# Kernel optimization log

Hardware: AMD Instinct MI355X
Metric: run time of the kernel (lower is better)

The kernel has to match this reference:

```python
import jax, jax.numpy as jnp
import numpy as np

N = 100000      # nodes
E = 1600000     # edges (avg degree 16)
B = 64          # graphs in batch
DIN = 128
HID = (256, 128, 64)
EPS = 1e-5


def _gcn(x, W, b, src, dst, n):
    # GCNConv: symmetric normalization with self-loops (already appended to src/dst)
    h = x @ W                                                   # [N, out]
    deg = jax.ops.segment_sum(jnp.ones_like(dst, dtype=h.dtype), dst, num_segments=n)
    dinv = jnp.where(deg > 0, jax.lax.rsqrt(jnp.maximum(deg, 1.0)), 0.0)
    norm = dinv[src] * dinv[dst]                                # [E+N]
    msg = h[src] * norm[:, None]                                # gather + scale
    return jax.ops.segment_sum(msg, dst, num_segments=n) + b    # scatter-add


def _bn(x, g, b):
    # BatchNorm1d over nodes (batch statistics, deterministic)
    mu = x.mean(0)
    var = x.var(0)
    return (x - mu) * jax.lax.rsqrt(var + EPS) * g + b


def setup_inputs():
    key = jax.random.key(0)
    ks = jax.random.split(key, 32)
    inp = {}
    inp["x"] = jax.random.normal(ks[0], (N, DIN), jnp.float32)
    inp["edge_index"] = jax.random.randint(ks[1], (2, E), 0, N, jnp.int32)
    inp["batch"] = jnp.sort(jax.random.randint(ks[2], (N,), 0, B, jnp.int32))
    dims = [DIN] + list(HID)
    for i in range(3):
        inp[f"W{i}"] = jax.random.normal(ks[3 + 4 * i], (dims[i], dims[i + 1]), jnp.float32) / np.sqrt(dims[i]).astype(np.float32)
        inp[f"b{i}"] = jnp.zeros((dims[i + 1],), jnp.float32)
        inp[f"g{i}"] = jnp.ones((dims[i + 1],), jnp.float32)
        inp[f"be{i}"] = jnp.zeros((dims[i + 1],), jnp.float32)
    d = HID[-1]
    inp["ln_g"] = jnp.ones((d,), jnp.float32)
    inp["ln_b"] = jnp.zeros((d,), jnp.float32)
    inp["att"] = jax.random.normal(ks[15], (d, 1), jnp.float32)
    mdims = [d, d // 2, d // 4, 2]
    for i in range(3):
        inp[f"M{i}W"] = jax.random.normal(ks[16 + 2 * i], (mdims[i], mdims[i + 1]), jnp.float32) / np.sqrt(mdims[i]).astype(np.float32)
        inp[f"M{i}b"] = jnp.zeros((mdims[i + 1],), jnp.float32)
    return inp


def reference(x, edge_index, batch, W0, b0, g0, be0, W1, b1, g1, be1, W2, b2, g2, be2,
              ln_g, ln_b, att, M0W, M0b, M1W, M1b, M2W, M2b):
    n = x.shape[0]
    loop = jnp.arange(n, dtype=edge_index.dtype)
    src = jnp.concatenate([edge_index[0], loop])
    dst = jnp.concatenate([edge_index[1], loop])
    for (W, b, g, be) in ((W0, b0, g0, be0), (W1, b1, g1, be1), (W2, b2, g2, be2)):
        x = jax.nn.relu(_bn(_gcn(x, W, b, src, dst, n), g, be))
    # LayerNorm over features
    mu = x.mean(-1, keepdims=True)
    var = x.var(-1, keepdims=True)
    x = (x - mu) * jax.lax.rsqrt(var + EPS) * ln_g + ln_b
    # global attention weights (softmax over ALL nodes, as in original code)
    aw = jax.nn.softmax(jnp.tanh(x @ att), axis=0)   # [N, 1]
    x = x * aw
    # global mean pool per graph
    s = jax.ops.segment_sum(x, batch, num_segments=B)
    cnt = jax.ops.segment_sum(jnp.ones((n, 1), x.dtype), batch, num_segments=B)
    pooled = s / jnp.maximum(cnt, 1.0)               # [B, 64]
    h = jax.nn.relu(pooled @ M0W + M0b)
    h = jax.nn.relu(h @ M1W + M1b)
    return h @ M2W + M2b                             # [B, 2]
```

## Files before the change

### kernel.cpp

```cpp
#include <hip/hip_runtime.h>
#include <hip/hip_bf16.h>
#include <cstdint>
#include <cstddef>

typedef float    f32x4  __attribute__((ext_vector_type(4)));
typedef __bf16   bf16x8 __attribute__((ext_vector_type(8)));
typedef _Float16 f16x4  __attribute__((ext_vector_type(4)));
typedef _Float16 f16x8  __attribute__((ext_vector_type(8)));

#define BN_G1 1024

__device__ __forceinline__ unsigned short f2bf(float x){
  unsigned u = __float_as_uint(x);
  return (unsigned short)((u + 0x7fffu + ((u >> 16) & 1u)) >> 16);
}
__device__ __forceinline__ float bfhi(unsigned short h){
  return __uint_as_float(((unsigned)h) << 16);
}

__global__ void k_deg_hist(const int* __restrict__ dst, int* __restrict__ deg, int E,
                           unsigned long long M){
  int f   = blockIdx.x & 7;
  int cid = blockIdx.x >> 3;
  int nch = gridDim.x >> 3;
  for(int i = cid*blockDim.x + threadIdx.x; i < E; i += nch*blockDim.x){
    int d = dst[i];
    int xf = (int)(((unsigned long long)(unsigned)d * M) >> 40);
    if(xf == f) atomicAdd(&deg[d], 1);
  }
}

__global__ void k_batch_hist(const int* __restrict__ batch, int* __restrict__ cnt, int n){
  __shared__ int h[64];
  if(threadIdx.x<64) h[threadIdx.x]=0;
  __syncthreads();
  int i = blockIdx.x*blockDim.x + threadIdx.x;
  int stride = gridDim.x*blockDim.x;
  for(; i<n; i+=stride) atomicAdd(&h[batch[i]], 1);
  __syncthreads();
  if(threadIdx.x<64 && h[threadIdx.x]) atomicAdd(&cnt[threadIdx.x], h[threadIdx.x]);
}

__global__ void k_dinv(const int* __restrict__ deg, float* __restrict__ dinv, int n){
  int i = blockIdx.x*blockDim.x + threadIdx.x;
  if(i<n) dinv[i] = rsqrtf((float)(deg[i]+1));
}

__global__ void k_scan1(const int* __restrict__ deg, int* __restrict__ bsum, int n){
  __shared__ int s[256];
  int base = blockIdx.x*1024 + threadIdx.x*4;
  int acc=0;
  #pragma unroll
  for(int j=0;j<4;j++){ int i=base+j; if(i<n) acc+=deg[i]; }
  s[threadIdx.x]=acc; __syncthreads();
  for(int off=128;off>0;off>>=1){
    if(threadIdx.x<off) s[threadIdx.x]+=s[threadIdx.x+off];
    __syncthreads();
  }
  if(threadIdx.x==0) bsum[blockIdx.x]=s[0];
}

__global__ void k_scan2(int* __restrict__ bsum, int nblk, int* __restrict__ rowptr, int n){
  __shared__ int s[128];
  int t=threadIdx.x;
  int v = (t<nblk)? bsum[t] : 0;
  s[t]=v; __syncthreads();
  for(int off=1; off<128; off<<=1){
    int a = (t>=off)? s[t-off] : 0;
    __syncthreads();
    s[t]+=a;
    __syncthreads();
  }
  if(t<nblk) bsum[t]=s[t]-v;
  if(t==127) rowptr[n]=s[127];
}

__global__ void k_scan3(const int* __restrict__ deg, const int* __restrict__ bsum,
                        int* __restrict__ rowptr, int* __restrict__ cursor, int n){
  __shared__ int s[256];
  int base = blockIdx.x*1024 + threadIdx.x*4;
  int v[4]; int acc=0;
  #pragma unroll
  for(int j=0;j<4;j++){ int i=base+j; v[j]=(i<n)?deg[i]:0; acc+=v[j]; }
  s[threadIdx.x]=acc; __syncthreads();
  for(int off=1; off<256; off<<=1){
    int a = (threadIdx.x>=off)? s[threadIdx.x-off] : 0;
    __syncthreads();
    s[threadIdx.x]+=a;
    __syncthreads();
  }
  int excl = s[threadIdx.x]-acc + bsum[blockIdx.x];
  #pragma unroll
  for(int j=0;j<4;j++){
    int i=base+j;
    if(i<n){ rowptr[i]=excl; cursor[i]=excl; excl+=v[j]; }
  }
}

__global__ void k_csr_fill(const int* __restrict__ src, const int* __restrict__ dst,
                           int* __restrict__ cursor, int* __restrict__ adj, int E,
                           unsigned long long M){
  int f   = blockIdx.x & 7;
  int cid = blockIdx.x >> 3;
  int nch = gridDim.x >> 3;
  for(int i = cid*blockDim.x + threadIdx.x; i < E; i += nch*blockDim.x){
    int d = dst[i];
    int xf = (int)(((unsigned long long)(unsigned)d * M) >> 40);
    if(xf == f){
      int p = atomicAdd(&cursor[d], 1);
      adj[p] = src[i];
    }
  }
}


__global__ void k_prep_w(const float* __restrict__ W, unsigned short* __restrict__ Wh,
                         unsigned short* __restrict__ Wl, int K, int F){
  int i = blockIdx.x*256 + threadIdx.x;
  if(i < K*F){
    int k = i / F, f = i % F;
    float a = W[i];
    unsigned short h = f2bf(a);
    Wh[(size_t)f*K + k] = h;
    Wl[(size_t)f*K + k] = f2bf(a - bfhi(h));
  }
}

__global__ void k_prep_x(const float* __restrict__ x, const float* __restrict__ dinv,
                         _Float16* __restrict__ x16, int n){
  int tid = blockIdx.x*256 + threadIdx.x;
  int node = tid >> 5;
  if(node>=n) return;
  int c4 = tid & 31;
  size_t idx = ((size_t)node<<5) + c4;
  float4 v = ((const float4*)x)[idx];
  float d = dinv[node];
  f16x4 o;
  o[0]=(_Float16)(v.x*d); o[1]=(_Float16)(v.y*d); o[2]=(_Float16)(v.z*d); o[3]=(_Float16)(v.w*d);
  ((f16x4*)x16)[idx] = o;
}

__global__ void k_agg16(const _Float16* __restrict__ zs, const int* __restrict__ rowptr,
                        const int* __restrict__ adj, const float* __restrict__ dinv,
                        const float* __restrict__ bias, _Float16* __restrict__ out,
                        int n, int lg8){
  int tid = blockIdx.x*blockDim.x + threadIdx.x;
  int node = tid >> lg8;
  if(node>=n) return;
  int c8 = tid & ((1<<lg8)-1);
  const f16x8* z8 = (const f16x8*)zs;
  size_t rb = ((size_t)node<<lg8) + c8;
  f16x8 self = z8[rb];
  float a0[8], a1[8], a2[8], a3[8];
  #pragma unroll
  for(int j=0;j<8;j++){ a0[j]=(float)self[j]; a1[j]=0.f; a2[j]=0.f; a3[j]=0.f; }
  int e = rowptr[node], end = rowptr[node+1];
  for(; e+3<end; e+=4){
    int s0=adj[e], s1=adj[e+1], s2=adj[e+2], s3=adj[e+3];
    f16x8 v0 = z8[((size_t)s0<<lg8)+c8];
    f16x8 v1 = z8[((size_t)s1<<lg8)+c8];
    f16x8 v2 = z8[((size_t)s2<<lg8)+c8];
    f16x8 v3 = z8[((size_t)s3<<lg8)+c8];
    #pragma unroll
    for(int j=0;j<8;j++){
      a0[j]+=(float)v0[j]; a1[j]+=(float)v1[j];
      a2[j]+=(float)v2[j]; a3[j]+=(float)v3[j];
    }
  }
  for(; e<end; e++){
    f16x8 v0 = z8[((size_t)adj[e]<<lg8)+c8];
    #pragma unroll
    for(int j=0;j<8;j++) a0[j]+=(float)v0[j];
  }
  float di = dinv[node];
  f16x8 o;
  #pragma unroll
  for(int j=0;j<8;j++){
    float r = ((a0[j]+a1[j])+(a2[j]+a3[j]))*di;
    if(bias) r += bias[(c8<<3)+j];
    o[j] = (_Float16)r;
  }
  ((f16x8*)out)[rb] = o;
}


template<typename AT> struct AFrag;
template<> struct AFrag<float>{
  float4 a,b;
  __device__ __forceinline__ void load(const float* p){ a=*(const float4*)p; b=*(const float4*)(p+4); }
  __device__ __forceinline__ void get(float o[8]) const {
    o[0]=a.x;o[1]=a.y;o[2]=a.z;o[3]=a.w;o[4]=b.x;o[5]=b.y;o[6]=b.z;o[7]=b.w;
  }
};
template<> struct AFrag<_Float16>{
  f16x8 v;
  __device__ __forceinline__ void load(const _Float16* p){ v=*(const f16x8*)p; }
  __device__ __forceinline__ void get(float o[8]) const {
    #pragma unroll
    for(int j=0;j<8;j++) o[j]=(float)v[j];
  }
};

template<int K, int F, bool BN, bool BIAS, bool RSC, typename AT, typename OT>
__global__ __launch_bounds__(256,2) void k_gemm_mfma(const AT* __restrict__ A,
    const unsigned short* __restrict__ Bh, const unsigned short* __restrict__ Bl,
    const float* __restrict__ sc, const float* __restrict__ sh,
    const float* __restrict__ bias, const float* __restrict__ rsc,
    OT* __restrict__ C, int n){
  constexpr int NF = F/16;
  __shared__ uint4 sBh[F*4];
  __shared__ uint4 sBl[F*4];
  const int l   = threadIdx.x & 63;
  const int w   = threadIdx.x >> 6;
  const int rlo = l & 15;
  const int khi = l >> 4;
  const int row0 = blockIdx.x*128 + w*32;

  f32x4 acc[2][NF];
  #pragma unroll
  for(int i=0;i<2;i++)
    #pragma unroll
    for(int j=0;j<NF;j++) acc[i][j] = (f32x4){0.f,0.f,0.f,0.f};

  const size_t e0 = (size_t)min(row0 + rlo,      n-1) * K + khi*8;
  const size_t e1 = (size_t)min(row0 + 16 + rlo, n-1) * K + khi*8;

  AFrag<AT> c0,c1,x0f,x1f;
  c0.load(A + e0); c1.load(A + e1);

  #pragma unroll 1
  for(int k0=0; k0<K; k0+=32){
    if(k0+32 < K){
      x0f.load(A + e0 + k0 + 32);
      x1f.load(A + e1 + k0 + 32);
    }
    __syncthreads();
    #pragma unroll
    for(int j=0;j<F/64;j++){
      int i  = threadIdx.x + j*256;
      int f  = i >> 2;
      int k8 = i & 3;
      int g  = ((f>>4)<<6) + (k8<<4) + (f&15);
      size_t goff = (size_t)f*K + k0 + (k8<<3);
      sBh[g] = *(const uint4*)(Bh + goff);
      sBl[g] = *(const uint4*)(Bl + goff);
    }
    float scr[8], shr[8];
    if(BN){
      float4 s0 = *(const float4*)(sc + k0 + khi*8);
      float4 s1 = *(const float4*)(sc + k0 + khi*8 + 4);
      float4 t0 = *(const float4*)(sh + k0 + khi*8);
      float4 t1 = *(const float4*)(sh + k0 + khi*8 + 4);
      scr[0]=s0.x;scr[1]=s0.y;scr[2]=s0.z;scr[3]=s0.w;scr[4]=s1.x;scr[5]=s1.y;scr[6]=s1.z;scr[7]=s1.w;
      shr[0]=t0.x;shr[1]=t0.y;shr[2]=t0.z;shr[3]=t0.w;shr[4]=t1.x;shr[5]=t1.y;shr[6]=t1.z;shr[7]=t1.w;
    }
    union { unsigned short u[8]; bf16x8 v; } H0,L0,H1,L1;
    {
      float v0[8], v1[8];
      c0.get(v0); c1.get(v1);
      #pragma unroll
      for(int j=0;j<8;j++){
        float y0 = v0[j], y1 = v1[j];
        if(BN){ y0 = fmaxf(fmaf(y0,scr[j],shr[j]),0.f); y1 = fmaxf(fmaf(y1,scr[j],shr[j]),0.f); }
        unsigned short h0 = f2bf(y0), h1 = f2bf(y1);
        H0.u[j]=h0; L0.u[j]=f2bf(y0 - bfhi(h0));
        H1.u[j]=h1; L1.u[j]=f2bf(y1 - bfhi(h1));
      }
    }
    bf16x8 ah0=H0.v, al0=L0.v, ah1=H1.v, al1=L1.v;
    __syncthreads();
    #pragma unroll
    for(int cf=0; cf<NF; cf++){
      bf16x8 bh = ((const bf16x8*)sBh)[cf*64 + l];
      bf16x8 bl = ((const bf16x8*)sBl)[cf*64 + l];
      acc[0][cf] = __builtin_amdgcn_mfma_f32_16x16x32_bf16(ah0, bh, acc[0][cf], 0,0,0);
      acc[1][cf] = __builtin_amdgcn_mfma_f32_16x16x32_bf16(ah1, bh, acc[1][cf], 0,0,0);
      acc[0][cf] = __builtin_amdgcn_mfma_f32_16x16x32_bf16(al0, bh, acc[0][cf], 0,0,0);
      acc[1][cf] = __builtin_amdgcn_mfma_f32_16x16x32_bf16(al1, bh, acc[1][cf], 0,0,0);
      acc[0][cf] = __builtin_amdgcn_mfma_f32_16x16x32_bf16(ah0, bl, acc[0][cf], 0,0,0);
      acc[1][cf] = __builtin_amdgcn_mfma_f32_16x16x32_bf16(ah1, bl, acc[1][cf], 0,0,0);
    }
    c0=x0f; c1=x1f;
  }

  #pragma unroll
  for(int rf=0; rf<2; rf++){
    #pragma unroll
    for(int r=0; r<4; r++){
      int m = row0 + rf*16 + khi*4 + r;
      if(m < n){
        float rs = RSC ? rsc[m] : 1.f;
        #pragma unroll
        for(int cf=0; cf<NF; cf++){
          int col = rlo + 16*cf;
          float v = acc[rf][cf][r];
          if(BIAS) v += bias[col];
          v *= rs;
          C[(size_t)m*F + col] = (OT)v;
        }
      }
    }
  }
}

__global__ __launch_bounds__(256) void k_bn_stats16(const _Float16* __restrict__ h,
                            float* __restrict__ partials, int n, int lgF){
  const int F   = 1 << lgF;
  const int C8  = 1 << (lgF-3);
  const int c8  = threadIdx.x & (C8-1);
  const int sub = threadIdx.x >> (lgF-3);
  const int rpb = 256 >> (lgF-3);
  float s[8], s2[8];
  #pragma unroll
  for(int j=0;j<8;j++){ s[j]=0.f; s2[j]=0.f; }
  for(int row = blockIdx.x*rpb + sub; row < n; row += gridDim.x*rpb){
    f16x8 v = ((const f16x8*)h)[(size_t)row*C8 + c8];
    #pragma unroll
    for(int j=0;j<8;j++){ float f=(float)v[j]; s[j]+=f; s2[j]=fmaf(f,f,s2[j]); }
  }
  __shared__ float rs [256*9];
  __shared__ float rs2[256*9];
  #pragma unroll
  for(int j=0;j<8;j++){ rs[threadIdx.x*9+j]=s[j]; rs2[threadIdx.x*9+j]=s2[j]; }
  __syncthreads();
  for(int half = rpb>>1; half>=1; half>>=1){
    if(sub < half){
      int o = (threadIdx.x + half*C8)*9;
      #pragma unroll
      for(int j=0;j<8;j++){ rs[threadIdx.x*9+j]+=rs[o+j]; rs2[threadIdx.x*9+j]+=rs2[o+j]; }
    }
    __syncthreads();
  }
  if(sub==0){
    float* p = partials + (size_t)blockIdx.x*(2*F);
    #pragma unroll
    for(int j=0;j<8;j++){
      p[c8*8+j]     = rs [threadIdx.x*9+j];
      p[F + c8*8+j] = rs2[threadIdx.x*9+j];
    }
  }
}

__global__ void k_bn_colsum(const float* __restrict__ partials, float* __restrict__ out, int F2){
  int c = blockIdx.x*64 + threadIdx.x;
  float s = 0.f;
  #pragma unroll 8
  for(int b=0; b<BN_G1; b++) s += partials[(size_t)b*F2 + c];
  out[c] = s;
}

__global__ void k_bn_finalize(const float* __restrict__ sums, const float* __restrict__ sumsq,
                              const float* __restrict__ g, const float* __restrict__ be,
                              float* __restrict__ scale, float* __restrict__ shift, int n, int F){
  int f = threadIdx.x;
  if(f<F){
    float mu = sums[f]/(float)n;
    float var = sumsq[f]/(float)n - mu*mu;
    float sc = g[f]*rsqrtf(var+1e-5f);
    scale[f] = sc;
    shift[f] = fmaf(-mu, sc, be[f]);
  }
}


__global__ void k_ln_att(const _Float16* __restrict__ x, const float* __restrict__ bsc, const float* __restrict__ bsh,
                         const float* __restrict__ g, const float* __restrict__ b,
                         const float* __restrict__ att, float* __restrict__ lnx, float* __restrict__ wv,
                         float* __restrict__ Ssum, int n){
  int lane = threadIdx.x & 63;
  int wid = (blockIdx.x<<2) + (threadIdx.x>>6);
  float gl=g[lane], bl=b[lane], al=att[lane];
  float scl=bsc[lane], shl=bsh[lane];
  float wacc=0.f;
  for(int node=wid; node<n; node+=4096){
    float raw = (float)x[((size_t)node<<6)+lane];
    float v = fmaxf(fmaf(raw, scl, shl), 0.f);
    float s=v;
    #pragma unroll
    for(int o=32;o>0;o>>=1) s += __shfl_xor(s,o);
    float mu = s*0.015625f;
    float d = v-mu;
    float q = d*d;
    #pragma unroll
    for(int o=32;o>0;o>>=1) q += __shfl_xor(q,o);
    float ln = d*rsqrtf(q*0.015625f + 1e-5f)*gl + bl;
    lnx[((size_t)node<<6)+lane] = ln;
    float a = ln*al;
    #pragma unroll
    for(int o=32;o>0;o>>=1) a += __shfl_xor(a,o);
    float wgt = expf(tanhf(a));
    if(lane==0) wv[node]=wgt;
    wacc += wgt;
  }
  __shared__ float sred[4];
  if(lane==0) sred[threadIdx.x>>6]=wacc;
  __syncthreads();
  if(threadIdx.x==0) atomicAdd(Ssum, sred[0]+sred[1]+sred[2]+sred[3]);
}

__global__ void k_pool(const float* __restrict__ lnx, const float* __restrict__ wv,
                       const int* __restrict__ batch, float* __restrict__ psum, int n){
  int lane = threadIdx.x & 63;
  int wave = threadIdx.x >> 6;
  int start = blockIdx.x*512 + wave*128;
  if(start >= n) return;
  int end = min(start+128, n);
  int cur = batch[start];
  float acc = 0.f;
  for(int i=start;i<end;i++){
    int bb = batch[i];
    if(bb != cur){ atomicAdd(&psum[cur*64+lane], acc); acc=0.f; cur=bb; }
    acc = fmaf(lnx[(size_t)i*64+lane], wv[i], acc);
  }
  atomicAdd(&psum[cur*64+lane], acc);
}

__global__ void k_mlp(const float* __restrict__ psum, const int* __restrict__ cnt,
                      const float* __restrict__ Ssum,
                      const float* __restrict__ M0W, const float* __restrict__ M0b,
                      const float* __restrict__ M1W, const float* __restrict__ M1b,
                      const float* __restrict__ M2W, const float* __restrict__ M2b,
                      float* __restrict__ out){
  int b = threadIdx.x;
  float S = Ssum[0];
  int cb = cnt[b]; if(cb<1) cb=1;
  float inv = 1.f/(S*(float)cb);
  float p[64];
  #pragma unroll
  for(int f=0;f<64;f++) p[f] = psum[b*64+f]*inv;
  float h1[32];
  #pragma unroll
  for(int j=0;j<32;j++){
    float a=M0b[j];
    #pragma unroll
    for(int f=0;f<64;f++) a = fmaf(p[f], M0W[f*32+j], a);
    h1[j]=fmaxf(a,0.f);
  }
  float h2[16];
  #pragma unroll
  for(int j=0;j<16;j++){
    float a=M1b[j];
    #pragma unroll
    for(int f=0;f<32;f++) a = fmaf(h1[f], M1W[f*16+j], a);
    h2[j]=fmaxf(a,0.f);
  }
  #pragma unroll
  for(int j=0;j<2;j++){
    float a=M2b[j];
    #pragma unroll
    for(int f=0;f<16;f++) a = fmaf(h2[f], M2W[f*2+j], a);
    out[b*2+j]=a;
  }
}


extern "C" void kernel_launch(void* const* d_in, const int* in_sizes, int n_in,
                              void* d_out, int out_size, void* d_ws, size_t ws_size,
                              hipStream_t stream){
  const float* x   = (const float*)d_in[0];
  const int*   ei  = (const int*)d_in[1];
  const int* batch = (const int*)d_in[2];
  const float* W0=(const float*)d_in[3],  *b0=(const float*)d_in[4],  *g0=(const float*)d_in[5],  *be0=(const float*)d_in[6];
  const float* W1=(const float*)d_in[7],  *b1=(const float*)d_in[8],  *g1=(const float*)d_in[9],  *be1=(const float*)d_in[10];
  const float* W2=(const float*)d_in[11], *b2=(const float*)d_in[12], *g2=(const float*)d_in[13], *be2=(const float*)d_in[14];
  const float* ln_g=(const float*)d_in[15], *ln_b=(const float*)d_in[16], *att=(const float*)d_in[17];
  const float* M0W=(const float*)d_in[18], *M0b=(const float*)d_in[19];
  const float* M1W=(const float*)d_in[20], *M1b=(const float*)d_in[21];
  const float* M2W=(const float*)d_in[22], *M2b=(const float*)d_in[23];
  const int N = in_sizes[0]/128;
  const int E = in_sizes[1]/2;
  const int* srcv = ei;
  const int* dstv = ei + E;
  const unsigned long long Mdiv = ((8ULL<<40) + (unsigned long long)N - 1) / (unsigned long long)N;

  char* base = (char*)d_ws;
  size_t off = 0;
  auto alloc = [&](size_t bytes)->char*{ char* p = base+off; off = (off+bytes+255)&~(size_t)255; return p; };
  int*   deg    = (int*)  alloc((size_t)N*4);
  int*   cnt    = (int*)  alloc(64*4);
  float* psum   = (float*)alloc(64*64*4);
  float* Ssum   = (float*)alloc(4);
  size_t zero_bytes = off;
  float* stats  = (float*)alloc(6*256*4);
  float* dinv   = (float*)alloc((size_t)N*4);
  int*   rowptr = (int*)  alloc(((size_t)N+1)*4);
  int*   cursor = (int*)  alloc((size_t)N*4);
  int*   bsum   = (int*)  alloc(128*4);
  float* bnsc   = (float*)alloc(3*256*4);
  float* bnsh   = (float*)alloc(3*256*4);
  float* partials = (float*)alloc((size_t)BN_G1*512*4);
  unsigned short* Wh0 = (unsigned short*)alloc((size_t)128*256*2);
  unsigned short* Wl0 = (unsigned short*)alloc((size_t)128*256*2);
  unsigned short* Wh1 = (unsigned short*)alloc((size_t)256*128*2);
  unsigned short* Wl1 = (unsigned short*)alloc((size_t)256*128*2);
  unsigned short* Wh2 = (unsigned short*)alloc((size_t)128*64*2);
  unsigned short* Wl2 = (unsigned short*)alloc((size_t)128*64*2);
  int*   adj    = (int*)  alloc((size_t)E*4);
  _Float16* x16 = (_Float16*)alloc((size_t)N*128*2);
  _Float16* R16 = (_Float16*)alloc((size_t)N*128*2);
  _Float16* P16 = (_Float16*)alloc((size_t)N*256*2);
  _Float16* Q16 = (_Float16*)alloc((size_t)N*128*2);
  _Float16* O16 = (_Float16*)alloc((size_t)N*64*2);
  float* LNX    = (float*)alloc((size_t)N*64*4);
  float* WV     = (float*)alloc((size_t)N*4);
  (void)ws_size; (void)n_in; (void)out_size;

  hipMemsetAsync(d_ws, 0, zero_bytes, stream);

  k_deg_hist  <<<2048,256,0,stream>>>(dstv, deg, E, Mdiv);
  k_batch_hist<<<256,256,0,stream>>>(batch, cnt, N);
  k_dinv      <<<(N+255)/256,256,0,stream>>>(deg, dinv, N);
  int nblk = (N+1023)/1024;
  k_scan1<<<nblk,256,0,stream>>>(deg, bsum, N);
  k_scan2<<<1,128,0,stream>>>(bsum, nblk, rowptr, N);
  k_scan3<<<nblk,256,0,stream>>>(deg, bsum, rowptr, cursor, N);
  k_csr_fill<<<2048,256,0,stream>>>(srcv, dstv, cursor, adj, E, Mdiv);
  k_prep_w<<<(128*256+255)/256,256,0,stream>>>(W0, Wh0, Wl0, 128, 256);
  k_prep_w<<<(256*128+255)/256,256,0,stream>>>(W1, Wh1, Wl1, 256, 128);
  k_prep_w<<<(128*64 +255)/256,256,0,stream>>>(W2, Wh2, Wl2, 128, 64);
  k_prep_x<<<(N*32+255)/256,256,0,stream>>>(x, dinv, x16, N);

  const int gemm_grid = (N+127)/128;

  k_agg16<<<(N*16+255)/256,256,0,stream>>>(x16, rowptr, adj, dinv, nullptr, R16, N, 4);
  k_gemm_mfma<128,256,false,true,false,_Float16,_Float16><<<gemm_grid,256,0,stream>>>(R16, Wh0, Wl0, nullptr,nullptr, b0, nullptr, P16, N);
  k_bn_stats16<<<BN_G1,256,0,stream>>>(P16, partials, N, 8);
  k_bn_colsum<<<512/64,64,0,stream>>>(partials, stats+0, 512);
  k_bn_finalize<<<1,256,0,stream>>>(stats+0, stats+256, g0, be0, bnsc+0, bnsh+0, N, 256);

  k_gemm_mfma<256,128,true,false,true,_Float16,_Float16><<<gemm_grid,256,0,stream>>>(P16, Wh1, Wl1, bnsc+0, bnsh+0, nullptr, dinv, Q16, N);
  k_agg16<<<(N*16+255)/256,256,0,stream>>>(Q16, rowptr, adj, dinv, b1, R16, N, 4);
  k_bn_stats16<<<BN_G1,256,0,stream>>>(R16, partials, N, 7);
  k_bn_colsum<<<256/64,64,0,stream>>>(partials, stats+512, 256);
  k_bn_finalize<<<1,256,0,stream>>>(stats+512, stats+640, g1, be1, bnsc+256, bnsh+256, N, 128);

  k_gemm_mfma<128,64,true,false,true,_Float16,_Float16><<<gemm_grid,256,0,stream>>>(R16, Wh2, Wl2, bnsc+256, bnsh+256, nullptr, dinv, Q16, N);
  k_agg16<<<(N*8+255)/256,256,0,stream>>>(Q16, rowptr, adj, dinv, b2, O16, N, 3);
  k_bn_stats16<<<BN_G1,256,0,stream>>>(O16, partials, N, 6);
  k_bn_colsum<<<128/64,64,0,stream>>>(partials, stats+1024, 128);
  k_bn_finalize<<<1,256,0,stream>>>(stats+1024, stats+1088, g2, be2, bnsc+512, bnsh+512, N, 64);

  k_ln_att<<<1024,256,0,stream>>>(O16, bnsc+512, bnsh+512, ln_g, ln_b, att, LNX, WV, Ssum, N);
  k_pool  <<<(N+511)/512,256,0,stream>>>(LNX, WV, batch, psum, N);
  k_mlp   <<<1,64,0,stream>>>(psum, cnt, Ssum, M0W,M0b,M1W,M1b,M2W,M2b, (float*)d_out);
}
```

Before: 685.7 us.

## Switch split GEMM to fp16 MFMA, fuse histogram, prep, BN-finalize and head kernels

Replaces the bf16 three-term split GEMM (hi*hi, lo*hi, hi*lo) with fp16 MFMA using only activation-hi times weight hi+lo, which drops the activation splitting and a third of the MFMAs. It also merges the degree and batch histograms, folds the dinv computation into the x prep, combines the three weight-prep launches, merges BN colsum and finalize, and fuses the LayerNorm/attention pass with pooling so the fp32 LNX intermediate is never written. This cuts launches and memory traffic. The cost is lower precision in the activation operand and a head kernel with fewer blocks and serial per-node shuffle reductions.

```diff
diff --git a/kernel.cpp b/kernel.cpp
--- a/kernel.cpp
+++ b/kernel.cpp
@@ -4,22 +4,17 @@
 #include <cstddef>
 
 typedef float    f32x4  __attribute__((ext_vector_type(4)));
-typedef __bf16   bf16x8 __attribute__((ext_vector_type(8)));
 typedef _Float16 f16x4  __attribute__((ext_vector_type(4)));
 typedef _Float16 f16x8  __attribute__((ext_vector_type(8)));
 
 #define BN_G1 1024
 
-__device__ __forceinline__ unsigned short f2bf(float x){
-  unsigned u = __float_as_uint(x);
-  return (unsigned short)((u + 0x7fffu + ((u >> 16) & 1u)) >> 16);
-}
-__device__ __forceinline__ float bfhi(unsigned short h){
-  return __uint_as_float(((unsigned)h) << 16);
-}
-
-__global__ void k_deg_hist(const int* __restrict__ dst, int* __restrict__ deg, int E,
-                           unsigned long long M){
+__global__ void k_hist(const int* __restrict__ dst, int* __restrict__ deg, int E,
+                       unsigned long long M,
+                       const int* __restrict__ batch, int* __restrict__ cnt, int n){
+  __shared__ int h[64];
+  if(threadIdx.x<64) h[threadIdx.x]=0;
+  __syncthreads();
   int f   = blockIdx.x & 7;
   int cid = blockIdx.x >> 3;
   int nch = gridDim.x >> 3;
@@ -28,22 +23,10 @@
     int xf = (int)(((unsigned long long)(unsigned)d * M) >> 40);
     if(xf == f) atomicAdd(&deg[d], 1);
   }
-}
-
-__global__ void k_batch_hist(const int* __restrict__ batch, int* __restrict__ cnt, int n){
-  __shared__ int h[64];
-  if(threadIdx.x<64) h[threadIdx.x]=0;
-  __syncthreads();
-  int i = blockIdx.x*blockDim.x + threadIdx.x;
-  int stride = gridDim.x*blockDim.x;
-  for(; i<n; i+=stride) atomicAdd(&h[batch[i]], 1);
+  for(int i = blockIdx.x*blockDim.x + threadIdx.x; i < n; i += gridDim.x*blockDim.x)
+    atomicAdd(&h[batch[i]], 1);
   __syncthreads();
   if(threadIdx.x<64 && h[threadIdx.x]) atomicAdd(&cnt[threadIdx.x], h[threadIdx.x]);
-}
-
-__global__ void k_dinv(const int* __restrict__ deg, float* __restrict__ dinv, int n){
-  int i = blockIdx.x*blockDim.x + threadIdx.x;
-  if(i<n) dinv[i] = rsqrtf((float)(deg[i]+1));
 }
 
 __global__ void k_scan1(const int* __restrict__ deg, int* __restrict__ bsum, int n){
@@ -114,27 +97,34 @@
 }
 
 
-__global__ void k_prep_w(const float* __restrict__ W, unsigned short* __restrict__ Wh,
-                         unsigned short* __restrict__ Wl, int K, int F){
+__global__ void k_prep_w3(const float* __restrict__ W0, const float* __restrict__ W1,
+                          const float* __restrict__ W2,
+                          _Float16* __restrict__ Wh0, _Float16* __restrict__ Wl0,
+                          _Float16* __restrict__ Wh1, _Float16* __restrict__ Wl1,
+                          _Float16* __restrict__ Wh2, _Float16* __restrict__ Wl2){
   int i = blockIdx.x*256 + threadIdx.x;
-  if(i < K*F){
-    int k = i / F, f = i % F;
-    float a = W[i];
-    unsigned short h = f2bf(a);
-    Wh[(size_t)f*K + k] = h;
-    Wl[(size_t)f*K + k] = f2bf(a - bfhi(h));
-  }
-}
-
-__global__ void k_prep_x(const float* __restrict__ x, const float* __restrict__ dinv,
-                         _Float16* __restrict__ x16, int n){
+  const float* W; _Float16 *Wh, *Wl; int K, F, idx;
+  if(i < 32768){        W=W0; Wh=Wh0; Wl=Wl0; K=128; F=256; idx=i; }
+  else if(i < 65536){   W=W1; Wh=Wh1; Wl=Wl1; K=256; F=128; idx=i-32768; }
+  else if(i < 73728){   W=W2; Wh=Wh2; Wl=Wl2; K=128; F=64;  idx=i-65536; }
+  else return;
+  int k = idx / F, f = idx % F;
+  float a = W[idx];
+  _Float16 h = (_Float16)a;
+  Wh[(size_t)f*K + k] = h;
+  Wl[(size_t)f*K + k] = (_Float16)(a - (float)h);
+}
+
+__global__ void k_prep_x(const float* __restrict__ x, const int* __restrict__ deg,
+                         float* __restrict__ dinv, _Float16* __restrict__ x16, int n){
   int tid = blockIdx.x*256 + threadIdx.x;
   int node = tid >> 5;
   if(node>=n) return;
   int c4 = tid & 31;
+  float d = rsqrtf((float)(deg[node]+1));
+  if(c4==0) dinv[node] = d;
   size_t idx = ((size_t)node<<5) + c4;
   float4 v = ((const float4*)x)[idx];
-  float d = dinv[node];
   f16x4 o;
   o[0]=(_Float16)(v.x*d); o[1]=(_Float16)(v.y*d); o[2]=(_Float16)(v.z*d); o[3]=(_Float16)(v.w*d);
   ((f16x4*)x16)[idx] = o;
@@ -183,30 +173,12 @@
   ((f16x8*)out)[rb] = o;
 }
 
-
-template<typename AT> struct AFrag;
-template<> struct AFrag<float>{
-  float4 a,b;
-  __device__ __forceinline__ void load(const float* p){ a=*(const float4*)p; b=*(const float4*)(p+4); }
-  __device__ __forceinline__ void get(float o[8]) const {
-    o[0]=a.x;o[1]=a.y;o[2]=a.z;o[3]=a.w;o[4]=b.x;o[5]=b.y;o[6]=b.z;o[7]=b.w;
-  }
-};
-template<> struct AFrag<_Float16>{
-  f16x8 v;
-  __device__ __forceinline__ void load(const _Float16* p){ v=*(const f16x8*)p; }
-  __device__ __forceinline__ void get(float o[8]) const {
-    #pragma unroll
-    for(int j=0;j<8;j++) o[j]=(float)v[j];
-  }
-};
-
-template<int K, int F, bool BN, bool BIAS, bool RSC, typename AT, typename OT>
-__global__ __launch_bounds__(256,2) void k_gemm_mfma(const AT* __restrict__ A,
-    const unsigned short* __restrict__ Bh, const unsigned short* __restrict__ Bl,
+template<int K, int F, bool BN, bool BIAS, bool RSC>
+__global__ __launch_bounds__(256,2) void k_gemm_mfma(const _Float16* __restrict__ A,
+    const _Float16* __restrict__ Bh, const _Float16* __restrict__ Bl,
     const float* __restrict__ sc, const float* __restrict__ sh,
     const float* __restrict__ bias, const float* __restrict__ rsc,
-    OT* __restrict__ C, int n){
+    _Float16* __restrict__ C, int n){
   constexpr int NF = F/16;
   __shared__ uint4 sBh[F*4];
   __shared__ uint4 sBl[F*4];
@@ -225,14 +197,15 @@
   const size_t e0 = (size_t)min(row0 + rlo,      n-1) * K + khi*8;
   const size_t e1 = (size_t)min(row0 + 16 + rlo, n-1) * K + khi*8;
 
-  AFrag<AT> c0,c1,x0f,x1f;
-  c0.load(A + e0); c1.load(A + e1);
+  f16x8 c0 = *(const f16x8*)(A + e0);
+  f16x8 c1 = *(const f16x8*)(A + e1);
+  f16x8 n0v, n1v;
 
   #pragma unroll 1
   for(int k0=0; k0<K; k0+=32){
     if(k0+32 < K){
-      x0f.load(A + e0 + k0 + 32);
-      x1f.load(A + e1 + k0 + 32);
+      n0v = *(const f16x8*)(A + e0 + k0 + 32);
+      n1v = *(const f16x8*)(A + e1 + k0 + 32);
     }
     __syncthreads();
     #pragma unroll
@@ -245,42 +218,34 @@
       sBh[g] = *(const uint4*)(Bh + goff);
       sBl[g] = *(const uint4*)(Bl + goff);
     }
-    float scr[8], shr[8];
+    f16x8 a0, a1;
     if(BN){
+      float scr[8], shr[8];
       float4 s0 = *(const float4*)(sc + k0 + khi*8);
       float4 s1 = *(const float4*)(sc + k0 + khi*8 + 4);
       float4 t0 = *(const float4*)(sh + k0 + khi*8);
       float4 t1 = *(const float4*)(sh + k0 + khi*8 + 4);
       scr[0]=s0.x;scr[1]=s0.y;scr[2]=s0.z;scr[3]=s0.w;scr[4]=s1.x;scr[5]=s1.y;scr[6]=s1.z;scr[7]=s1.w;
       shr[0]=t0.x;shr[1]=t0.y;shr[2]=t0.z;shr[3]=t0.w;shr[4]=t1.x;shr[5]=t1.y;shr[6]=t1.z;shr[7]=t1.w;
-    }
-    union { unsigned short u[8]; bf16x8 v; } H0,L0,H1,L1;
-    {
-      float v0[8], v1[8];
-      c0.get(v0); c1.get(v1);
       #pragma unroll
       for(int j=0;j<8;j++){
-        float y0 = v0[j], y1 = v1[j];
-        if(BN){ y0 = fmaxf(fmaf(y0,scr[j],shr[j]),0.f); y1 = fmaxf(fmaf(y1,scr[j],shr[j]),0.f); }
-        unsigned short h0 = f2bf(y0), h1 = f2bf(y1);
-        H0.u[j]=h0; L0.u[j]=f2bf(y0 - bfhi(h0));
-        H1.u[j]=h1; L1.u[j]=f2bf(y1 - bfhi(h1));
+        a0[j] = (_Float16)fmaxf(fmaf((float)c0[j],scr[j],shr[j]),0.f);
+        a1[j] = (_Float16)fmaxf(fmaf((float)c1[j],scr[j],shr[j]),0.f);
       }
-    }
-    bf16x8 ah0=H0.v, al0=L0.v, ah1=H1.v, al1=L1.v;
+    }else{
+      a0 = c0; a1 = c1;
+    }
     __syncthreads();
     #pragma unroll
     for(int cf=0; cf<NF; cf++){
-      bf16x8 bh = ((const bf16x8*)sBh)[cf*64 + l];
-      bf16x8 bl = ((const bf16x8*)sBl)[cf*64 + l];
-      acc[0][cf] = __builtin_amdgcn_mfma_f32_16x16x32_bf16(ah0, bh, acc[0][cf], 0,0,0);
-      acc[1][cf] = __builtin_amdgcn_mfma_f32_16x16x32_bf16(ah1, bh, acc[1][cf], 0,0,0);
-      acc[0][cf] = __builtin_amdgcn_mfma_f32_16x16x32_bf16(al0, bh, acc[0][cf], 0,0,0);
-      acc[1][cf] = __builtin_amdgcn_mfma_f32_16x16x32_bf16(al1, bh, acc[1][cf], 0,0,0);
-      acc[0][cf] = __builtin_amdgcn_mfma_f32_16x16x32_bf16(ah0, bl, acc[0][cf], 0,0,0);
-      acc[1][cf] = __builtin_amdgcn_mfma_f32_16x16x32_bf16(ah1, bl, acc[1][cf], 0,0,0);
-    }
-    c0=x0f; c1=x1f;
+      f16x8 bh = ((const f16x8*)sBh)[cf*64 + l];
+      f16x8 bl = ((const f16x8*)sBl)[cf*64 + l];
+      acc[0][cf] = __builtin_amdgcn_mfma_f32_16x16x32_f16(a0, bh, acc[0][cf], 0,0,0);
+      acc[1][cf] = __builtin_amdgcn_mfma_f32_16x16x32_f16(a1, bh, acc[1][cf], 0,0,0);
+      acc[0][cf] = __builtin_amdgcn_mfma_f32_16x16x32_f16(a0, bl, acc[0][cf], 0,0,0);
+      acc[1][cf] = __builtin_amdgcn_mfma_f32_16x16x32_f16(a1, bl, acc[1][cf], 0,0,0);
+    }
+    c0=n0v; c1=n1v;
   }
 
   #pragma unroll
@@ -296,7 +261,7 @@
           float v = acc[rf][cf][r];
           if(BIAS) v += bias[col];
           v *= rs;
-          C[(size_t)m*F + col] = (OT)v;
+          C[(size_t)m*F + col] = (_Float16)v;
         }
       }
     }
@@ -341,78 +306,66 @@
   }
 }
 
-__global__ void k_bn_colsum(const float* __restrict__ partials, float* __restrict__ out, int F2){
+__global__ void k_bn_fin2(const float* __restrict__ partials, int F,
+                          const float* __restrict__ g, const float* __restrict__ be,
+                          float* __restrict__ scale, float* __restrict__ shift, int n){
   int c = blockIdx.x*64 + threadIdx.x;
-  float s = 0.f;
+  float s=0.f, s2=0.f;
   #pragma unroll 8
-  for(int b=0; b<BN_G1; b++) s += partials[(size_t)b*F2 + c];
-  out[c] = s;
-}
-
-__global__ void k_bn_finalize(const float* __restrict__ sums, const float* __restrict__ sumsq,
-                              const float* __restrict__ g, const float* __restrict__ be,
-                              float* __restrict__ scale, float* __restrict__ shift, int n, int F){
-  int f = threadIdx.x;
-  if(f<F){
-    float mu = sums[f]/(float)n;
-    float var = sumsq[f]/(float)n - mu*mu;
-    float sc = g[f]*rsqrtf(var+1e-5f);
-    scale[f] = sc;
-    shift[f] = fmaf(-mu, sc, be[f]);
-  }
-}
-
-
-__global__ void k_ln_att(const _Float16* __restrict__ x, const float* __restrict__ bsc, const float* __restrict__ bsh,
-                         const float* __restrict__ g, const float* __restrict__ b,
-                         const float* __restrict__ att, float* __restrict__ lnx, float* __restrict__ wv,
-                         float* __restrict__ Ssum, int n){
-  int lane = threadIdx.x & 63;
-  int wid = (blockIdx.x<<2) + (threadIdx.x>>6);
-  float gl=g[lane], bl=b[lane], al=att[lane];
-  float scl=bsc[lane], shl=bsh[lane];
-  float wacc=0.f;
-  for(int node=wid; node<n; node+=4096){
-    float raw = (float)x[((size_t)node<<6)+lane];
-    float v = fmaxf(fmaf(raw, scl, shl), 0.f);
-    float s=v;
-    #pragma unroll
-    for(int o=32;o>0;o>>=1) s += __shfl_xor(s,o);
-    float mu = s*0.015625f;
-    float d = v-mu;
-    float q = d*d;
-    #pragma unroll
-    for(int o=32;o>0;o>>=1) q += __shfl_xor(q,o);
-    float ln = d*rsqrtf(q*0.015625f + 1e-5f)*gl + bl;
-    lnx[((size_t)node<<6)+lane] = ln;
-    float a = ln*al;
-    #pragma unroll
-    for(int o=32;o>0;o>>=1) a += __shfl_xor(a,o);
-    float wgt = expf(tanhf(a));
-    if(lane==0) wv[node]=wgt;
-    wacc += wgt;
-  }
-  __shared__ float sred[4];
-  if(lane==0) sred[threadIdx.x>>6]=wacc;
-  __syncthreads();
-  if(threadIdx.x==0) atomicAdd(Ssum, sred[0]+sred[1]+sred[2]+sred[3]);
-}
-
-__global__ void k_pool(const float* __restrict__ lnx, const float* __restrict__ wv,
-                       const int* __restrict__ batch, float* __restrict__ psum, int n){
+  for(int b=0; b<BN_G1; b++){
+    const float* p = partials + (size_t)b*2*F;
+    s  += p[c];
+    s2 += p[F + c];
+  }
+  float mu = s/(float)n;
+  float var = s2/(float)n - mu*mu;
+  float sc = g[c]*rsqrtf(var+1e-5f);
+  scale[c] = sc;
+  shift[c] = fmaf(-mu, sc, be[c]);
+}
+
+__global__ void k_head(const _Float16* __restrict__ x, const float* __restrict__ bsc,
+                       const float* __restrict__ bsh, const float* __restrict__ g,
+                       const float* __restrict__ b, const float* __restrict__ att,
+                       const int* __restrict__ batch, float* __restrict__ psum,
+                       float* __restrict__ Ssum, int n){
   int lane = threadIdx.x & 63;
   int wave = threadIdx.x >> 6;
   int start = blockIdx.x*512 + wave*128;
-  if(start >= n) return;
-  int end = min(start+128, n);
-  int cur = batch[start];
-  float acc = 0.f;
-  for(int i=start;i<end;i++){
-    int bb = batch[i];
-    if(bb != cur){ atomicAdd(&psum[cur*64+lane], acc); acc=0.f; cur=bb; }
-    acc = fmaf(lnx[(size_t)i*64+lane], wv[i], acc);
-  }
-  atomicAdd(&psum[cur*64+lane], acc);
+  __shared__ float sred[4];
+  float wacc = 0.f;
+  if(start < n){
+    int end = min(start+128, n);
+    float gl=g[lane], bl=b[lane], al=att[lane];
+    float scl=bsc[lane], shl=bsh[lane];
+    int cur = batch[start];
+    float acc = 0.f;
+    for(int i=start;i<end;i++){
+      float raw = (float)x[(size_t)i*64+lane];
+      float v = fmaxf(fmaf(raw, scl, shl), 0.f);
+      float s=v;
+      #pragma unroll
+      for(int o=32;o>0;o>>=1) s += __shfl_xor(s,o);
+      float mu = s*0.015625f;
+      float d = v-mu;
+      float q = d*d;
+      #pragma unroll
+      for(int o=32;o>0;o>>=1) q += __shfl_xor(q,o);
+      float ln = d*rsqrtf(q*0.015625f + 1e-5f)*gl + bl;
+      float a = ln*al;
+      #pragma unroll
+      for(int o=32;o>0;o>>=1) a += __shfl_xor(a,o);
+      float wgt = expf(tanhf(a));
+      int bb = batch[i];
+      if(bb != cur){ atomicAdd(&psum[cur*64+lane], acc); acc=0.f; cur=bb; }
+      acc = fmaf(ln, wgt, acc);
+      wacc += wgt;
+    }
+    atomicAdd(&psum[cur*64+lane], acc);
+  }
+  if(lane==0) sred[wave] = (start<n)? wacc : 0.f;
+  __syncthreads();
+  if(threadIdx.x==0) atomicAdd(Ssum, sred[0]+sred[1]+sred[2]+sred[3]);
 }
 
 __global__ void k_mlp(const float* __restrict__ psum, const int* __restrict__ cnt,
@@ -481,7 +434,6 @@
   float* psum   = (float*)alloc(64*64*4);
   float* Ssum   = (float*)alloc(4);
   size_t zero_bytes = off;
-  float* stats  = (float*)alloc(6*256*4);
   float* dinv   = (float*)alloc((size_t)N*4);
   int*   rowptr = (int*)  alloc(((size_t)N+1)*4);
   int*   cursor = (int*)  alloc((size_t)N*4);
@@ -489,58 +441,48 @@
   float* bnsc   = (float*)alloc(3*256*4);
   float* bnsh   = (float*)alloc(3*256*4);
   float* partials = (float*)alloc((size_t)BN_G1*512*4);
-  unsigned short* Wh0 = (unsigned short*)alloc((size_t)128*256*2);
-  unsigned short* Wl0 = (unsigned short*)alloc((size_t)128*256*2);
-  unsigned short* Wh1 = (unsigned short*)alloc((size_t)256*128*2);
-  unsigned short* Wl1 = (unsigned short*)alloc((size_t)256*128*2);
-  unsigned short* Wh2 = (unsigned short*)alloc((size_t)128*64*2);
-  unsigned short* Wl2 = (unsigned short*)alloc((size_t)128*64*2);
+  _Float16* Wh0 = (_Float16*)alloc((size_t)128*256*2);
+  _Float16* Wl0 = (_Float16*)alloc((size_t)128*256*2);
+  _Float16* Wh1 = (_Float16*)alloc((size_t)256*128*2);
+  _Float16* Wl1 = (_Float16*)alloc((size_t)256*128*2);
+  _Float16* Wh2 = (_Float16*)alloc((size_t)128*64*2);
+  _Float16* Wl2 = (_Float16*)alloc((size_t)128*64*2);
   int*   adj    = (int*)  alloc((size_t)E*4);
   _Float16* x16 = (_Float16*)alloc((size_t)N*128*2);
   _Float16* R16 = (_Float16*)alloc((size_t)N*128*2);
   _Float16* P16 = (_Float16*)alloc((size_t)N*256*2);
   _Float16* Q16 = (_Float16*)alloc((size_t)N*128*2);
   _Float16* O16 = (_Float16*)alloc((size_t)N*64*2);
-  float* LNX    = (float*)alloc((size_t)N*64*4);
-  float* WV     = (float*)alloc((size_t)N*4);
   (void)ws_size; (void)n_in; (void)out_size;
 
   hipMemsetAsync(d_ws, 0, zero_bytes, stream);
 
-  k_deg_hist  <<<2048,256,0,stream>>>(dstv, deg, E, Mdiv);
-  k_batch_hist<<<256,256,0,stream>>>(batch, cnt, N);
-  k_dinv      <<<(N+255)/256,256,0,stream>>>(deg, dinv, N);
+  k_hist <<<2048,256,0,stream>>>(dstv, deg, E, Mdiv, batch, cnt, N);
   int nblk = (N+1023)/1024;
   k_scan1<<<nblk,256,0,stream>>>(deg, bsum, N);
   k_scan2<<<1,128,0,stream>>>(bsum, nblk, rowptr, N);
   k_scan3<<<nblk,256,0,stream>>>(deg, bsum, rowptr, cursor, N);
   k_csr_fill<<<2048,256,0,stream>>>(srcv, dstv, cursor, adj, E, Mdiv);
-  k_prep_w<<<(128*256+255)/256,256,0,stream>>>(W0, Wh0, Wl0, 128, 256);
-  k_prep_w<<<(256*128+255)/256,256,0,stream>>>(W1, Wh1, Wl1, 256, 128);
-  k_prep_w<<<(128*64 +255)/256,256,0,stream>>>(W2, Wh2, Wl2, 128, 64);
-  k_prep_x<<<(N*32+255)/256,256,0,stream>>>(x, dinv, x16, N);
+  k_prep_w3<<<288,256,0,stream>>>(W0,W1,W2, Wh0,Wl0, Wh1,Wl1, Wh2,Wl2);
+  k_prep_x<<<(N*32+255)/256,256,0,stream>>>(x, deg, dinv, x16, N);
 
   const int gemm_grid = (N+127)/128;
 
   k_agg16<<<(N*16+255)/256,256,0,stream>>>(x16, rowptr, adj, dinv, nullptr, R16, N, 4);
-  k_gemm_mfma<128,256,false,true,false,_Float16,_Float16><<<gemm_grid,256,0,stream>>>(R16, Wh0, Wl0, nullptr,nullptr, b0, nullptr, P16, N);
+  k_gemm_mfma<128,256,false,true,false><<<gemm_grid,256,0,stream>>>(R16, Wh0, Wl0, nullptr,nullptr, b0, nullptr, P16, N);
   k_bn_stats16<<<BN_G1,256,0,stream>>>(P16, partials, N, 8);
-  k_bn_colsum<<<512/64,64,0,stream>>>(partials, stats+0, 512);
-  k_bn_finalize<<<1,256,0,stream>>>(stats+0, stats+256, g0, be0, bnsc+0, bnsh+0, N, 256);
-
-  k_gemm_mfma<256,128,true,false,true,_Float16,_Float16><<<gemm_grid,256,0,stream>>>(P16, Wh1, Wl1, bnsc+0, bnsh+0, nullptr, dinv, Q16, N);
+  k_bn_fin2<<<4,64,0,stream>>>(partials, 256, g0, be0, bnsc+0, bnsh+0, N);
+
+  k_gemm_mfma<256,128,true,false,true><<<gemm_grid,256,0,stream>>>(P16, Wh1, Wl1, bnsc+0, bnsh+0, nullptr, dinv, Q16, N);
   k_agg16<<<(N*16+255)/256,256,0,stream>>>(Q16, rowptr, adj, dinv, b1, R16, N, 4);
   k_bn_stats16<<<BN_G1,256,0,stream>>>(R16, partials, N, 7);
-  k_bn_colsum<<<256/64,64,0,stream>>>(partials, stats+512, 256);
-  k_bn_finalize<<<1,256,0,stream>>>(stats+512, stats+640, g1, be1, bnsc+256, bnsh+256, N, 128);
-
-  k_gemm_mfma<128,64,true,false,true,_Float16,_Float16><<<gemm_grid,256,0,stream>>>(R16, Wh2, Wl2, bnsc+256, bnsh+256, nullptr, dinv, Q16, N);
+  k_bn_fin2<<<2,64,0,stream>>>(partials, 128, g1, be1, bnsc+256, bnsh+256, N);
+
+  k_gemm_mfma<128,64,true,false,true><<<gemm_grid,256,0,stream>>>(R16, Wh2, Wl2, bnsc+256, bnsh+256, nullptr, dinv, Q16, N);
   k_agg16<<<(N*8+255)/256,256,0,stream>>>(Q16, rowptr, adj, dinv, b2, O16, N, 3);
   k_bn_stats16<<<BN_G1,256,0,stream>>>(O16, partials, N, 6);
-  k_bn_colsum<<<128/64,64,0,stream>>>(partials, stats+1024, 128);
-  k_bn_finalize<<<1,256,0,stream>>>(stats+1024, stats+1088, g2, be2, bnsc+512, bnsh+512, N, 64);
-
-  k_ln_att<<<1024,256,0,stream>>>(O16, bnsc+512, bnsh+512, ln_g, ln_b, att, LNX, WV, Ssum, N);
-  k_pool  <<<(N+511)/512,256,0,stream>>>(LNX, WV, batch, psum, N);
-  k_mlp   <<<1,64,0,stream>>>(psum, cnt, Ssum, M0W,M0b,M1W,M1b,M2W,M2b, (float*)d_out);
-}
+  k_bn_fin2<<<1,64,0,stream>>>(partials, 64, g2, be2, bnsc+512, bnsh+512, N);
+
+  k_head<<<(N+511)/512,256,0,stream>>>(O16, bnsc+512, bnsh+512, ln_g, ln_b, att, batch, psum, Ssum, N);
+  k_mlp <<<1,64,0,stream>>>(psum, cnt, Ssum, M0W,M0b,M1W,M1b,M2W,M2b, (float*)d_out);
+}
```

Measured after the change: 735.5 us. +7.3%, slower.
